# Optimization experiments

Hardware: AMD Instinct MI355X
Metric: run time of the kernel (lower is better)

## Reference

```python
import jax, jax.numpy as jnp
import numpy as np

N_HEAD = 16
DROP_P = 0.1


def setup_inputs() -> dict:
    key = jax.random.key(0)
    ks = jax.random.split(key, 5)
    B, T, C = 2, 2048, 1024
    return {
        "x": jax.random.normal(ks[0], (B, T, C), dtype=jnp.float32),
        "w_attn": jax.random.normal(ks[1], (C, 3 * C), dtype=jnp.float32) * 0.02,
        "b_attn": jax.random.normal(ks[2], (3 * C,), dtype=jnp.float32) * 0.02,
        "w_proj": jax.random.normal(ks[3], (C, C), dtype=jnp.float32) * 0.02,
        "b_proj": jax.random.normal(ks[4], (C,), dtype=jnp.float32) * 0.02,
    }


def reference(x, w_attn, b_attn, w_proj, b_proj):
    B, T, C = x.shape
    H = N_HEAD
    D = C // H  # head dim
    qkv = x @ w_attn + b_attn                      # [B,T,3C]
    q, k, v = jnp.split(qkv, 3, axis=-1)
    # [B,T,C] -> [B,H,T,D]
    q = q.reshape(B, T, H, D).transpose(0, 2, 1, 3)
    k = k.reshape(B, T, H, D).transpose(0, 2, 1, 3)
    v = v.reshape(B, T, H, D).transpose(0, 2, 1, 3)
    scale = 1.0 / jnp.sqrt(jnp.float32(D))
    attn = jnp.einsum("bhqd,bhkd->bhqk", q, k) * scale  # [B,H,T,T]
    causal = jnp.tril(jnp.ones((T, T), dtype=bool))
    attn = jnp.where(causal[None, None], attn, jnp.float32(-jnp.inf))
    attn = jax.nn.softmax(attn, axis=-1)
    # dropout p=0.1 (training mode in original); deterministic fixed key here
    keep = jax.random.bernoulli(jax.random.key(42), 1.0 - DROP_P, attn.shape)
    attn = jnp.where(keep, attn / (1.0 - DROP_P), 0.0)
    out = jnp.einsum("bhqk,bhkd->bhqd", attn, v)   # [B,H,T,D]
    out = out.transpose(0, 2, 1, 3).reshape(B, T, C)
    return out @ w_proj + b_proj
```

## Files before the change

### kernel.cpp

```cpp
#include <hip/hip_runtime.h>
#include <hip/hip_bf16.h>
#include <stdint.h>
#include <math.h>

#define TSEQ   2048
#define NBATCH 2
#define NHEAD  16
#define HDIM   64
#define CDIM   1024

#define KEEP_LIMIT 3865470464u
#define QSC 0.18033688011112042f

typedef short  bf16x8 __attribute__((ext_vector_type(8)));
typedef float  f32x4  __attribute__((ext_vector_type(4)));

__device__ __forceinline__ float fast_exp2(float x) {
    float r; asm("v_exp_f32 %0, %1" : "=v"(r) : "v"(x)); return r;
}
__device__ __forceinline__ uint32_t cvt_pk_bf16(float a, float b) {
    uint32_t r; asm("v_cvt_pk_bf16_f32 %0, %1, %2" : "=v"(r) : "v"(a), "v"(b)); return r;
}

__device__ __forceinline__ uint32_t rotl32(uint32_t x, int r) {
    return __builtin_amdgcn_alignbit(x, x, 32 - r);
}

__device__ __forceinline__ uint32_t tf2x32_xor(uint32_t x0, uint32_t x1) {
    const uint32_t ka = 0u, kb = 42u;
    const uint32_t kc = ka ^ kb ^ 0x1BD11BDAu;
    x0 += ka; x1 += kb;
#define TFR(r) { x0 += x1; x1 = rotl32(x1, r); x1 ^= x0; }
    TFR(13) TFR(15) TFR(26) TFR(6)
    x0 += kb; x1 += kc + 1u;
    TFR(17) TFR(29) TFR(16) TFR(24)
    x0 += kc; x1 += ka + 2u;
    TFR(13) TFR(15) TFR(26) TFR(6)
    x0 += ka; x1 += kb + 3u;
    TFR(17) TFR(29) TFR(16) TFR(24)
    x0 += kb; x1 += kc + 4u;
    TFR(13) TFR(15) TFR(26) TFR(6)
    x0 += kc; x1 += ka + 5u;
#undef TFR
    return x0 ^ x1;
}

__device__ __forceinline__ bool tf_keep(uint32_t idx) {
    return tf2x32_xor(0u, idx) < KEEP_LIMIT;
}

__device__ __forceinline__ float bf2f(ushort u) {
    union { uint32_t i; float f; } c; c.i = ((uint32_t)u) << 16; return c.f;
}

__device__ __forceinline__ void async_copy16(void* lds, const void* g) {
    __builtin_amdgcn_global_load_lds(
        (const __attribute__((address_space(1))) unsigned int*)g,
        (__attribute__((address_space(3))) unsigned int*)lds, 16, 0, 0);
}

__global__ __launch_bounds__(256) void cvt_bf16(
    const float* __restrict__ src, ushort* __restrict__ dst, int n)
{
    int idx = (blockIdx.x * 256 + threadIdx.x) * 8;
    if (idx >= n) return;
    float4 a = *(const float4*)(src + idx);
    float4 b = *(const float4*)(src + idx + 4);
    uint4 o;
    o.x = cvt_pk_bf16(a.x, a.y); o.y = cvt_pk_bf16(a.z, a.w);
    o.z = cvt_pk_bf16(b.x, b.y); o.w = cvt_pk_bf16(b.z, b.w);
    *(uint4*)(dst + idx) = o;
}

__global__ __launch_bounds__(256) void transpose_cvt(
    const float* __restrict__ src, ushort* __restrict__ dst, int K, int N)
{
    __shared__ float t[32][33];
    const int n0 = blockIdx.x * 32, k0 = blockIdx.y * 32;
    const int i = threadIdx.x;
    {
        int k = i >> 3, n4 = (i & 7) * 4;
        float4 v = *(const float4*)(src + (size_t)(k0 + k) * N + n0 + n4);
        t[k][n4 + 0] = v.x; t[k][n4 + 1] = v.y; t[k][n4 + 2] = v.z; t[k][n4 + 3] = v.w;
    }
    __syncthreads();
    {
        int n = i >> 3, k4 = (i & 7) * 4;
        uint2 o;
        o.x = cvt_pk_bf16(t[k4 + 0][n], t[k4 + 1][n]);
        o.y = cvt_pk_bf16(t[k4 + 2][n], t[k4 + 3][n]);
        *(uint2*)(dst + (size_t)(n0 + n) * K + k0 + k4) = o;
    }
}

template<int MODE>
__global__ __launch_bounds__(256) void gemm_bf16(
    const ushort* __restrict__ A, const ushort* __restrict__ Bt,
    const float* __restrict__ bias,
    ushort* __restrict__ Q, ushort* __restrict__ Kq, ushort* __restrict__ V,
    float* __restrict__ Cf, int M, int N, int K)
{
    __shared__ ushort As[2][128 * 32];
    __shared__ ushort Bs[2][128 * 32];
    const int tid = threadIdx.x, lane = tid & 63, wid = tid >> 6;
    const int l15 = lane & 15, l4 = lane >> 4;
    const int wr = wid >> 1, wc = wid & 1;
    const int bn = blockIdx.x, bm = blockIdx.y;
    const int NTK = K >> 5;

    f32x4 acc[4][4];
#pragma unroll
    for (int m = 0; m < 4; ++m)
#pragma unroll
        for (int n = 0; n < 4; ++n) acc[m][n] = (f32x4){0.f, 0.f, 0.f, 0.f};

    auto stage = [&](int p, int k0) {
#pragma unroll
        for (int j = 0; j < 2; ++j) {
            const int rbase = wid * 32 + j * 16;
            const int row = rbase + (lane >> 2);
            const ushort* src = A + (size_t)(bm * 128 + row) * K + k0 + (lane & 3) * 8;
            async_copy16(&As[p][rbase * 32], src);
        }
#pragma unroll
        for (int j = 0; j < 2; ++j) {
            const int rbase = wid * 32 + j * 16;
            const int row = rbase + (lane >> 2);
            const ushort* src = Bt + (size_t)(bn * 128 + row) * K + k0 + (lane & 3) * 8;
            async_copy16(&Bs[p][rbase * 32], src);
        }
    };
    auto compute = [&](int p) {
        bf16x8 af[4], bf[4];
#pragma unroll
        for (int m = 0; m < 4; ++m)
            af[m] = *(const bf16x8*)&As[p][(wr * 64 + m * 16 + l15) * 32 + l4 * 8];
#pragma unroll
        for (int n = 0; n < 4; ++n)
            bf[n] = *(const bf16x8*)&Bs[p][(wc * 64 + n * 16 + l15) * 32 + l4 * 8];
#pragma unroll
        for (int m = 0; m < 4; ++m)
#pragma unroll
            for (int n = 0; n < 4; ++n)
                acc[m][n] = __builtin_amdgcn_mfma_f32_16x16x32_bf16(af[m], bf[n], acc[m][n], 0, 0, 0);
    };

    stage(0, 0);
    __syncthreads();
    for (int t = 0; t < NTK; ++t) {
        const int p = t & 1;
        if (t + 1 < NTK) stage(p ^ 1, (t + 1) << 5);
        compute(p);
        __syncthreads();
    }

    const int colbase = bn * 128 + wc * 64;
    const int rowbase = bm * 128 + wr * 64;
    if (MODE == 0) {
#pragma unroll
        for (int n = 0; n < 4; ++n) {
            const int col = colbase + n * 16 + l15;
            const float bv = bias[col];
#pragma unroll
            for (int m = 0; m < 4; ++m)
#pragma unroll
                for (int r = 0; r < 4; ++r) {
                    const int row = rowbase + m * 16 + l4 * 4 + r;
                    Cf[(size_t)row * N + col] = acc[m][n][r] + bv;
                }
        }
    } else {
#pragma unroll
        for (int n = 0; n < 4; ++n) {
            const int col = colbase + n * 16 + l15;
            const int which = col >> 10, cc = col & 1023;
            const int hh = cc >> 6, dd = cc & 63;
            const float bv = bias[col];
            const float sc = (which == 0) ? QSC : 1.0f;
#pragma unroll
            for (int m = 0; m < 4; ++m) {
                float v0 = (acc[m][n][0] + bv) * sc, v1 = (acc[m][n][1] + bv) * sc;
                float v2 = (acc[m][n][2] + bv) * sc, v3 = (acc[m][n][3] + bv) * sc;
                uint32_t pk01 = cvt_pk_bf16(v0, v1), pk23 = cvt_pk_bf16(v2, v3);
                ushort vals[4] = { (ushort)pk01, (ushort)(pk01 >> 16),
                                   (ushort)pk23, (ushort)(pk23 >> 16) };
#pragma unroll
                for (int r = 0; r < 4; ++r) {
                    const int row = rowbase + m * 16 + l4 * 4 + r;
                    const int bb = row >> 11, tt = row & 2047;
                    if (which == 0)
                        Q[(((size_t)(bb * NHEAD + hh)) * TSEQ + tt) * HDIM + dd] = vals[r];
                    else if (which == 1)
                        Kq[(((size_t)(bb * NHEAD + hh)) * TSEQ + tt) * HDIM + dd] = vals[r];
                    else
                        V[(((size_t)(bb * NHEAD + hh)) * HDIM + dd) * TSEQ + tt] = vals[r];
                }
            }
        }
    }
}

__global__ __launch_bounds__(256) void attn_fwd_mfma(
    const ushort* __restrict__ Qb, const ushort* __restrict__ Kb,
    const ushort* __restrict__ VbT,
    ushort* __restrict__ Ap, float* __restrict__ mp, float* __restrict__ lp)
{
    __shared__ ushort Ks[2][64 * 64];
    __shared__ ushort Vt[2][64 * 64];
    __shared__ ushort Ps[64 * 64];
    const int tid = threadIdx.x;
    const int lane = tid & 63;
    const int wid = tid >> 6;
    const int l15 = lane & 15, l4 = lane >> 4;
    const int pair = blockIdx.x >> 1, half = blockIdx.x & 1;
    const int h = blockIdx.y, b = blockIdx.z;
    const int hb = b * NHEAD + h;
    const size_t headoff = (size_t)hb * TSEQ * HDIM;
    const ushort* Qg = Qb + headoff;
    const ushort* Kg = Kb + headoff;
    const ushort* Vg = VbT + headoff;

    auto stage = [&](int p, int kt) {
        const ushort* Kt = Kg + (size_t)(kt * 64) * HDIM;
        const ushort* Vt0 = Vg + kt * 64;
#pragma unroll
        for (int c = 0; c < 2; ++c) {
            const int rbase = wid * 16 + c * 8;
            const int row = rbase + (lane >> 3);
            const ushort* srcK = Kt + row * 64 + (((lane & 7) * 8) ^ ((row & 7) << 3));
            async_copy16(&Ks[p][rbase * 64], srcK);
            const ushort* srcV = Vt0 + (size_t)row * TSEQ + (((lane & 7) * 8) ^ ((row & 7) << 3));
            async_copy16(&Vt[p][rbase * 64], srcV);
        }
    };

    const int swq = (l15 & 7) << 3;
    const int prow = wid * 16 + l15;

    for (int pass = 0; pass < 2; ++pass) {
        const int qt = pass ? (TSEQ / 64 - 1) - pair : pair;
        const int ntk = qt + 1;
        const int kb = half ? (ntk + 1) >> 1 : 0;
        const int ke = half ? ntk : (ntk + 1) >> 1;
        const int pidx = (hb * 32 + qt) * 2 + half;
        const int tilerow = wid * 16 + l15;
        ushort* arow = Ap + (size_t)pidx * 4096 + tilerow * 64;

        if (kb >= ke) {
#pragma unroll
            for (int dt = 0; dt < 4; ++dt) {
                ushort4 z; z.x = z.y = z.z = z.w = 0;
                *(ushort4*)&arow[dt * 16 + l4 * 4] = z;
            }
            if (l4 == 0) { mp[pidx * 64 + tilerow] = -INFINITY; lp[pidx * 64 + tilerow] = 0.f; }
            continue;
        }

        const int qglob = qt * 64 + tilerow;
        bf16x8 qf0, qf1;
        {
            const ushort* qrow = Qg + (size_t)qglob * HDIM;
            qf0 = *(const bf16x8*)(qrow + l4 * 8);
            qf1 = *(const bf16x8*)(qrow + 32 + l4 * 8);
        }

        f32x4 oacc[4];
#pragma unroll
        for (int i = 0; i < 4; ++i) oacc[i] = (f32x4){0.f, 0.f, 0.f, 0.f};
        float mi = -INFINITY, li = 0.f;
        const uint32_t rowbase = ((uint32_t)hb * TSEQ + (uint32_t)qglob) * TSEQ;

        stage(0, kb);
        __syncthreads();

        for (int kt = kb; kt < ke; ++kt) {
            const int p = (kt - kb) & 1;
            if (kt + 1 < ke) stage(p ^ 1, kt + 1);

            f32x4 s4[4];
#pragma unroll
            for (int ct = 0; ct < 4; ++ct) {
                const int krow = ct * 16 + l15;
                const int sw = (krow & 7) << 3;
                bf16x8 kf0 = *(const bf16x8*)&Ks[p][krow * 64 + ((l4 * 8) ^ sw)];
                bf16x8 kf1 = *(const bf16x8*)&Ks[p][krow * 64 + ((l4 * 8 + 32) ^ sw)];
                f32x4 a = {0.f, 0.f, 0.f, 0.f};
                a = __builtin_amdgcn_mfma_f32_16x16x32_bf16(kf0, qf0, a, 0, 0, 0);
                a = __builtin_amdgcn_mfma_f32_16x16x32_bf16(kf1, qf1, a, 0, 0, 0);
                s4[ct] = a;
            }

            const int kb0 = kt * 64;
            float ev[4][4];
            if (kt == qt) {
#pragma unroll
                for (int ct = 0; ct < 4; ++ct)
#pragma unroll
                    for (int r = 0; r < 4; ++r) {
                        const int kglob = kb0 + ct * 16 + l4 * 4 + r;
                        ev[ct][r] = (kglob <= qglob) ? s4[ct][r] : -INFINITY;
                    }
            } else {
#pragma unroll
                for (int ct = 0; ct < 4; ++ct)
#pragma unroll
                    for (int r = 0; r < 4; ++r) ev[ct][r] = s4[ct][r];
            }
            float mx;
            {
                float t0 = fmaxf(fmaxf(ev[0][0], ev[0][1]), ev[0][2]);
                float t1 = fmaxf(fmaxf(ev[0][3], ev[1][0]), ev[1][1]);
                float t2 = fmaxf(fmaxf(ev[1][2], ev[1][3]), ev[2][0]);
                float t3 = fmaxf(fmaxf(ev[2][1], ev[2][2]), ev[2][3]);
                float t4 = fmaxf(fmaxf(ev[3][0], ev[3][1]), ev[3][2]);
                float t5 = fmaxf(fmaxf(t0, t1), ev[3][3]);
                float t6 = fmaxf(fmaxf(t2, t3), t4);
                mx = fmaxf(t5, t6);
            }
            mx = fmaxf(mx, __shfl_xor(mx, 16));
            mx = fmaxf(mx, __shfl_xor(mx, 32));

            if (__any(mx > mi)) {
                const float mnew = fmaxf(mi, mx);
                const float alpha = fast_exp2(mi - mnew);
                mi = mnew;
                li *= alpha;
#pragma unroll
                for (int dt = 0; dt < 4; ++dt) {
                    oacc[dt][0] *= alpha; oacc[dt][1] *= alpha;
                    oacc[dt][2] *= alpha; oacc[dt][3] *= alpha;
                }
            }
            float rs = 0.f;
#pragma unroll
            for (int ct = 0; ct < 4; ++ct)
#pragma unroll
                for (int r = 0; r < 4; ++r) {
                    ev[ct][r] = fast_exp2(ev[ct][r] - mi);
                    rs += ev[ct][r];
                }
            rs += __shfl_xor(rs, 16);
            rs += __shfl_xor(rs, 32);
            li += rs;

            const uint32_t idx0 = rowbase + (uint32_t)kb0;
#pragma unroll
            for (int ct = 0; ct < 4; ++ct) {
                const uint32_t kk = idx0 + (uint32_t)(ct * 16 + l4 * 4);
                const float p0 = tf_keep(kk + 0u) ? ev[ct][0] : 0.f;
                const float p1 = tf_keep(kk + 1u) ? ev[ct][1] : 0.f;
                const float p2 = tf_keep(kk + 2u) ? ev[ct][2] : 0.f;
                const float p3 = tf_keep(kk + 3u) ? ev[ct][3] : 0.f;
                uint2 pk;
                pk.x = cvt_pk_bf16(p0, p1);
                pk.y = cvt_pk_bf16(p2, p3);
                *(uint2*)&Ps[prow * 64 + ((ct * 16 + l4 * 4) ^ swq)] = pk;
            }

            bf16x8 pf0 = *(const bf16x8*)&Ps[prow * 64 + ((l4 * 8) ^ swq)];
            bf16x8 pf1 = *(const bf16x8*)&Ps[prow * 64 + ((l4 * 8 + 32) ^ swq)];
#pragma unroll
            for (int dt = 0; dt < 4; ++dt) {
                const int drow = dt * 16 + l15;
                const int swv = (drow & 7) << 3;
                bf16x8 vf0 = *(const bf16x8*)&Vt[p][drow * 64 + ((l4 * 8) ^ swv)];
                bf16x8 vf1 = *(const bf16x8*)&Vt[p][drow * 64 + ((l4 * 8 + 32) ^ swv)];
                oacc[dt] = __builtin_amdgcn_mfma_f32_16x16x32_bf16(vf0, pf0, oacc[dt], 0, 0, 0);
                oacc[dt] = __builtin_amdgcn_mfma_f32_16x16x32_bf16(vf1, pf1, oacc[dt], 0, 0, 0);
            }
            __syncthreads();
        }

#pragma unroll
        for (int dt = 0; dt < 4; ++dt) {
            uint2 o;
            o.x = cvt_pk_bf16(oacc[dt][0], oacc[dt][1]);
            o.y = cvt_pk_bf16(oacc[dt][2], oacc[dt][3]);
            *(uint2*)&arow[dt * 16 + l4 * 4] = o;
        }
        if (l4 == 0) { mp[pidx * 64 + tilerow] = mi; lp[pidx * 64 + tilerow] = li; }
    }
}

__global__ __launch_bounds__(256) void attn_merge(
    const ushort* __restrict__ Ap, const float* __restrict__ mp,
    const float* __restrict__ lp, ushort* __restrict__ AO)
{
    const int gidx = blockIdx.x * 16 + (threadIdx.x >> 4);
    const int hb = gidx >> 11;
    const int q  = gidx & 2047;
    const int qt = q >> 6, row = q & 63;
    const int sub = (threadIdx.x & 15) * 4;
    const int pidx0 = (hb * 32 + qt) * 2;
    const int pr = pidx0 * 64 + row;
    const float m0 = mp[pr], m1 = mp[pr + 64];
    const float l0 = lp[pr], l1 = lp[pr + 64];
    const float m  = fmaxf(m0, m1);
    const float w0 = fast_exp2(m0 - m), w1 = fast_exp2(m1 - m);
    const float inv = 1.0f / ((l0 * w0 + l1 * w1) * 0.9f);
    const float s0 = w0 * inv, s1 = w1 * inv;
    ushort4 a0 = *(const ushort4*)&Ap[(size_t)pidx0 * 4096 + row * 64 + sub];
    ushort4 a1 = *(const ushort4*)&Ap[(size_t)(pidx0 + 1) * 4096 + row * 64 + sub];
    const int b = hb >> 4, h = hb & 15;
    ushort* orow = AO + ((size_t)(b * TSEQ + q)) * CDIM + h * HDIM + sub;
    uint2 o;
    o.x = cvt_pk_bf16(bf2f(a0.x) * s0 + bf2f(a1.x) * s1,
                      bf2f(a0.y) * s0 + bf2f(a1.y) * s1);
    o.y = cvt_pk_bf16(bf2f(a0.z) * s0 + bf2f(a1.z) * s1,
                      bf2f(a0.w) * s0 + bf2f(a1.w) * s1);
    *(uint2*)orow = o;
}

extern "C" void kernel_launch(void* const* d_in, const int* in_sizes, int n_in,
                              void* d_out, int out_size, void* d_ws, size_t ws_size,
                              hipStream_t stream)
{
    const float* x      = (const float*)d_in[0];
    const float* w_attn = (const float*)d_in[1];
    const float* b_attn = (const float*)d_in[2];
    const float* w_proj = (const float*)d_in[3];
    const float* b_proj = (const float*)d_in[4];
    float* out = (float*)d_out;

    const size_t NH = (size_t)NBATCH * NHEAD * TSEQ * HDIM;
    ushort* Qb  = (ushort*)d_ws;
    ushort* Kb  = Qb + NH;
    ushort* VbT = Kb + NH;
    ushort* AO  = VbT + NH;
    ushort* xb  = AO + NH;
    ushort* wTa = xb + NH;
    ushort* wTp = wTa + (size_t)3072 * 1024;
    float*  mp  = (float*)(wTp + (size_t)1024 * 1024);
    float*  lp  = mp + (size_t)2048 * 64;

    ushort* Aparts = (ushort*)d_out;

    cvt_bf16<<<2048, 256, 0, stream>>>(x, xb, 4096 * 1024);
    transpose_cvt<<<dim3(96, 32), 256, 0, stream>>>(w_attn, wTa, 1024, 3072);
    transpose_cvt<<<dim3(32, 32), 256, 0, stream>>>(w_proj, wTp, 1024, 1024);

    gemm_bf16<1><<<dim3(24, 32), 256, 0, stream>>>(
        xb, wTa, b_attn, Qb, Kb, VbT, nullptr, 4096, 3072, 1024);

    attn_fwd_mfma<<<dim3(32, NHEAD, NBATCH), 256, 0, stream>>>(
        Qb, Kb, VbT, Aparts, mp, lp);

    attn_merge<<<4096, 256, 0, stream>>>(Aparts, mp, lp, AO);

    gemm_bf16<0><<<dim3(8, 32), 256, 0, stream>>>(
        AO, wTp, b_proj, nullptr, nullptr, nullptr, out, 4096, 1024, 1024);
}
```

Before: 236.0 us.

## Single-buffer K tile and hoist dropout hash before QK MFMAs

K shared memory goes from double-buffered to single-buffered, and the next K tile's async load now starts after an extra barrier placed right after the QK^T MFMAs. V stays double-buffered. The Threefry dropout hashes for each tile are computed before the QK MFMAs so the integer ALU work can overlap the matrix-core work and the K loads. This lowers LDS use, which may raise occupancy, but adds a barrier per iteration and keeps 16 hash values live in registers.

After: 237.4 us. About the same (+0.6%).

```diff
diff --git a/kernel.cpp b/kernel.cpp
--- a/kernel.cpp
+++ b/kernel.cpp
@@ -45,10 +45,6 @@
     return x0 ^ x1;
 }
 
-__device__ __forceinline__ bool tf_keep(uint32_t idx) {
-    return tf2x32_xor(0u, idx) < KEEP_LIMIT;
-}
-
 __device__ __forceinline__ float bf2f(ushort u) {
     union { uint32_t i; float f; } c; c.i = ((uint32_t)u) << 16; return c.f;
 }
@@ -205,7 +201,7 @@
     const ushort* __restrict__ VbT,
     ushort* __restrict__ Ap, float* __restrict__ mp, float* __restrict__ lp)
 {
-    __shared__ ushort Ks[2][64 * 64];
+    __shared__ ushort Ks[64 * 64];
     __shared__ ushort Vt[2][64 * 64];
     __shared__ ushort Ps[64 * 64];
     const int tid = threadIdx.x;
@@ -220,15 +216,22 @@
     const ushort* Kg = Kb + headoff;
     const ushort* Vg = VbT + headoff;
 
-    auto stage = [&](int p, int kt) {
+    auto stageK = [&](int kt) {
         const ushort* Kt = Kg + (size_t)(kt * 64) * HDIM;
-        const ushort* Vt0 = Vg + kt * 64;
 #pragma unroll
         for (int c = 0; c < 2; ++c) {
             const int rbase = wid * 16 + c * 8;
             const int row = rbase + (lane >> 3);
             const ushort* srcK = Kt + row * 64 + (((lane & 7) * 8) ^ ((row & 7) << 3));
-            async_copy16(&Ks[p][rbase * 64], srcK);
+            async_copy16(&Ks[rbase * 64], srcK);
+        }
+    };
+    auto stageV = [&](int p, int kt) {
+        const ushort* Vt0 = Vg + kt * 64;
+#pragma unroll
+        for (int c = 0; c < 2; ++c) {
+            const int rbase = wid * 16 + c * 8;
+            const int row = rbase + (lane >> 3);
             const ushort* srcV = Vt0 + (size_t)row * TSEQ + (((lane & 7) * 8) ^ ((row & 7) << 3));
             async_copy16(&Vt[p][rbase * 64], srcV);
         }
@@ -270,27 +273,42 @@
         float mi = -INFINITY, li = 0.f;
         const uint32_t rowbase = ((uint32_t)hb * TSEQ + (uint32_t)qglob) * TSEQ;
 
-        stage(0, kb);
+        stageK(kb);
+        stageV(0, kb);
         __syncthreads();
 
         for (int kt = kb; kt < ke; ++kt) {
             const int p = (kt - kb) & 1;
-            if (kt + 1 < ke) stage(p ^ 1, kt + 1);
+            const bool pf = (kt + 1 < ke);
+            if (pf) stageV(p ^ 1, kt + 1);
+
+            const int kb0 = kt * 64;
+            const uint32_t idx0 = rowbase + (uint32_t)kb0;
+            uint32_t tfb[4][4];
+#pragma unroll
+            for (int ct = 0; ct < 4; ++ct) {
+                const uint32_t kk = idx0 + (uint32_t)(ct * 16 + l4 * 4);
+                tfb[ct][0] = tf2x32_xor(0u, kk + 0u);
+                tfb[ct][1] = tf2x32_xor(0u, kk + 1u);
+                tfb[ct][2] = tf2x32_xor(0u, kk + 2u);
+                tfb[ct][3] = tf2x32_xor(0u, kk + 3u);
+            }
 
             f32x4 s4[4];
 #pragma unroll
             for (int ct = 0; ct < 4; ++ct) {
                 const int krow = ct * 16 + l15;
                 const int sw = (krow & 7) << 3;
-                bf16x8 kf0 = *(const bf16x8*)&Ks[p][krow * 64 + ((l4 * 8) ^ sw)];
-                bf16x8 kf1 = *(const bf16x8*)&Ks[p][krow * 64 + ((l4 * 8 + 32) ^ sw)];
+                bf16x8 kf0 = *(const bf16x8*)&Ks[krow * 64 + ((l4 * 8) ^ sw)];
+                bf16x8 kf1 = *(const bf16x8*)&Ks[krow * 64 + ((l4 * 8 + 32) ^ sw)];
                 f32x4 a = {0.f, 0.f, 0.f, 0.f};
                 a = __builtin_amdgcn_mfma_f32_16x16x32_bf16(kf0, qf0, a, 0, 0, 0);
                 a = __builtin_amdgcn_mfma_f32_16x16x32_bf16(kf1, qf1, a, 0, 0, 0);
                 s4[ct] = a;
             }
-
-            const int kb0 = kt * 64;
+            __syncthreads();
+            if (pf) stageK(kt + 1);
+
             float ev[4][4];
             if (kt == qt) {
 #pragma unroll
@@ -343,14 +361,12 @@
             rs += __shfl_xor(rs, 32);
             li += rs;
 
-            const uint32_t idx0 = rowbase + (uint32_t)kb0;
 #pragma unroll
             for (int ct = 0; ct < 4; ++ct) {
-                const uint32_t kk = idx0 + (uint32_t)(ct * 16 + l4 * 4);
-                const float p0 = tf_keep(kk + 0u) ? ev[ct][0] : 0.f;
-                const float p1 = tf_keep(kk + 1u) ? ev[ct][1] : 0.f;
-                const float p2 = tf_keep(kk + 2u) ? ev[ct][2] : 0.f;
-                const float p3 = tf_keep(kk + 3u) ? ev[ct][3] : 0.f;
+                const float p0 = (tfb[ct][0] < KEEP_LIMIT) ? ev[ct][0] : 0.f;
+                const float p1 = (tfb[ct][1] < KEEP_LIMIT) ? ev[ct][1] : 0.f;
+                const float p2 = (tfb[ct][2] < KEEP_LIMIT) ? ev[ct][2] : 0.f;
+                const float p3 = (tfb[ct][3] < KEEP_LIMIT) ? ev[ct][3] : 0.f;
                 uint2 pk;
                 pk.x = cvt_pk_bf16(p0, p1);
                 pk.y = cvt_pk_bf16(p2, p3);
```
